# Performance work log

Hardware: AMD Instinct MI355X
Metric: run time of the kernel (lower is better)

The kernel has to match this reference:

```python
import jax, jax.numpy as jnp
import numpy as np

CUBOID = (2, 7, 7)
SHIFT = (1, 3, 3)
NUM_HEADS = 4
LN_EPS = 1e-5


def _cuboid_reorder(data, cs):
    # (B,T,H,W,C) -> (B, num_cuboids, cuboid_volume, C), strategy = ('l','l','l')
    B, T, H, W, C = data.shape
    bt, bh, bw = cs
    d = data.reshape(B, T // bt, bt, H // bh, bh, W // bw, bw, C)
    d = d.transpose(0, 1, 3, 5, 2, 4, 6, 7)
    return d.reshape(B, (T // bt) * (H // bh) * (W // bw), bt * bh * bw, C)


def _cuboid_reorder_reverse(data, cs, shape):
    T, H, W = shape
    bt, bh, bw = cs
    B, _, _, C = data.shape
    d = data.reshape(B, T // bt, H // bh, W // bw, bt, bh, bw, C)
    d = d.transpose(0, 1, 4, 2, 5, 3, 6, 7)
    return d.reshape(B, T, H, W, C)


def _compute_attn_mask(shape, cs, ss):
    # Shift-window mask; no padding needed (dims divisible by cuboid), so the
    # data mask is all-ones and the mask is just the shift-region equality mask.
    T, H, W = shape
    shift_mask = np.zeros((1, T, H, W, 1), np.float32)
    cnt = 0
    for t in (slice(-cs[0]), slice(-cs[0], -ss[0]), slice(-ss[0], None)):
        for h in (slice(-cs[1]), slice(-cs[1], -ss[1]), slice(-ss[1], None)):
            for w in (slice(-cs[2]), slice(-cs[2], -ss[2]), slice(-ss[2], None)):
                shift_mask[:, t, h, w, :] = cnt
                cnt += 1
    sm = _cuboid_reorder(shift_mask, cs)[0, :, :, 0]  # (num_cuboids, vol)
    attn_mask = (sm[:, None, :] - sm[:, :, None]) == 0  # (num_cuboids, vol, vol)
    return jnp.asarray(attn_mask)


def setup_inputs() -> dict:
    key = jax.random.key(0)
    k1, k2, k3 = jax.random.split(key, 3)
    B, T, H, W, C = 2, 16, 56, 56, 128
    return {
        "x": jax.random.normal(k1, (B, T, H, W, C), jnp.float32),
        "gamma": jnp.ones((C,), jnp.float32),
        "beta": jnp.zeros((C,), jnp.float32),
        "w_qkv": jax.random.normal(k2, (C, 3 * C), jnp.float32) * 0.05,
        "w_proj": jax.random.normal(k3, (C, C), jnp.float32) * 0.05,
        "b_proj": jnp.zeros((C,), jnp.float32),
    }


def reference(x, gamma, beta, w_qkv, w_proj, b_proj):
    B, T, H, W, C = x.shape
    hd = C // NUM_HEADS
    scale = hd ** -0.5

    # pre-norm (torch LayerNorm, biased variance)
    mu = jnp.mean(x, axis=-1, keepdims=True)
    var = jnp.var(x, axis=-1, keepdims=True)
    xn = (x - mu) * jax.lax.rsqrt(var + LN_EPS) * gamma + beta

    # shift + cuboid reorder
    shifted = jnp.roll(xn, shift=(-SHIFT[0], -SHIFT[1], -SHIFT[2]), axis=(1, 2, 3))
    r = _cuboid_reorder(shifted, CUBOID)  # (B, nc, vol, C)
    nc, vol = r.shape[1], r.shape[2]

    qkv = (r @ w_qkv).reshape(B, nc, vol, 3, NUM_HEADS, hd)
    q = qkv[..., 0, :, :] * scale  # (B, nc, vol, h, d)
    k = qkv[..., 1, :, :]
    v = qkv[..., 2, :, :]

    attn_score = jnp.einsum("bnihd,bnjhd->bhnij", q, k)  # (B, h, nc, vol, vol)
    mask = _compute_attn_mask((T, H, W), CUBOID, SHIFT)  # (nc, vol, vol)
    attn_score = jnp.where(mask[None, None], attn_score, jnp.float32(-1e18))
    attn = jax.nn.softmax(attn_score, axis=-1) * mask[None, None]

    out = jnp.einsum("bhnij,bnjhd->bnihd", attn, v).reshape(B, nc, vol, C)
    out = out @ w_proj + b_proj

    out = _cuboid_reorder_reverse(out, CUBOID, (T, H, W))
    out = jnp.roll(out, shift=SHIFT, axis=(1, 2, 3))
    return out
```

## Files before the change

### kernel.cpp

```cpp
#include <hip/hip_runtime.h>

typedef short s16x8 __attribute__((ext_vector_type(8)));
typedef float f32x4_t __attribute__((ext_vector_type(4)));

#define VOL 98
#define VPAD 112
#define CH 128
#define NWV 7
#define NTH (NWV * 64)
#define MASKNEG -1e9f

struct Smem {
  unsigned short bufA[VPAD * CH];
  unsigned short vt[CH * CH];
  unsigned short pst[NWV][512];
  unsigned int catbits[27][4];
  int cat[VPAD];
  int gidx[VPAD];
};

__device__ __forceinline__ unsigned short f2bf(float f) {
  unsigned int u = __float_as_uint(f);
  unsigned int r = u + 0x7FFFu + ((u >> 16) & 1u);
  return (unsigned short)(r >> 16);
}
__device__ __forceinline__ unsigned int pk2(float a, float b) {
  return (unsigned int)f2bf(a) | ((unsigned int)f2bf(b) << 16);
}
__device__ __forceinline__ int swz(int row, int colEl, int strideB) {
  return (row * strideB + colEl * 2) ^ ((row & 7) << 4);
}
__device__ __forceinline__ s16x8 ldsRd(const unsigned short* buf, int row, int colEl, int strideB) {
  return *(const s16x8*)((const char*)buf + swz(row, colEl, strideB));
}
__device__ __forceinline__ void ldsWr64(unsigned short* buf, int row, int colEl, int strideB,
                                        unsigned int lo, unsigned int hi) {
  unsigned long long v = (unsigned long long)lo | ((unsigned long long)hi << 32);
  *(unsigned long long*)((char*)buf + swz(row, colEl, strideB)) = v;
}
__device__ __forceinline__ void ldsWr128(unsigned short* buf, int row, int colEl, int strideB, uint4 v) {
  *(uint4*)((char*)buf + swz(row, colEl, strideB)) = v;
}
__device__ __forceinline__ s16x8 u4cast(unsigned a, unsigned b, unsigned c, unsigned d) {
  union { uint4 u; s16x8 v; } cv;
  cv.u = make_uint4(a, b, c, d);
  return cv.v;
}

__global__ void prepack_weights(const float* __restrict__ wqkv,
                                const float* __restrict__ wproj,
                                unsigned short* __restrict__ dst) {
  int lane = threadIdx.x;
  int blk = blockIdx.x;
  if (blk < 96) {
    int ct = blk >> 2, ks = blk & 3;
    int r0 = ks * 32 + ((lane >> 4) << 3);
    int col = ct * 16 + (lane & 15);
    unsigned short* d = dst + (((size_t)(ct * 4 + ks) * 64 + lane) * 8);
#pragma unroll
    for (int j = 0; j < 8; ++j) d[j] = f2bf(wqkv[(size_t)(r0 + j) * 384 + col]);
  } else {
    int bb = blk - 96;
    int ct = bb >> 2, ks = bb & 3;
    int r0 = ks * 32 + ((lane >> 4) << 3);
    int col = ct * 16 + (lane & 15);
    unsigned short* d = dst + 49152 + (((size_t)(ct * 4 + ks) * 64 + lane) * 8);
#pragma unroll
    for (int j = 0; j < 8; ++j) d[j] = f2bf(wproj[(size_t)(r0 + j) * 128 + col]);
  }
}

__global__ __launch_bounds__(NTH, 4) void fused_cuboid_attn(
    const float* __restrict__ x, const float* __restrict__ gamma,
    const float* __restrict__ beta, const float* __restrict__ bproj,
    const unsigned short* __restrict__ wfrag, float* __restrict__ out) {
  __shared__ Smem s;
  const int tid = threadIdx.x;
  const int lane = tid & 63;
  const int itw = tid >> 6;
  const int l15 = lane & 15;
  const int lg = lane >> 4;
  const int lg4 = lg * 4;
  const int lg8 = lg * 8;
  const int bid = blockIdx.x;
  const int b = bid >> 9;
  const int n = bid & 511;
  const int nt = n >> 6, nh = (n >> 3) & 7, nw = n & 7;

  {
    uint4 z = make_uint4(0, 0, 0, 0);
    uint4* pv = (uint4*)s.vt;
    for (int i = tid; i < 2048; i += NTH) pv[i] = z;
    if (tid < 224) ((uint4*)(s.bufA + 98 * CH))[tid] = z;
    if (tid < 27) ((uint4*)s.catbits)[tid] = z;
    if (tid >= NTH - (VPAD - VOL)) s.cat[VOL + tid - (NTH - (VPAD - VOL))] = -1;
  }
  __syncthreads();

  {
    const int grp = tid >> 4;
    const int l = tid & 15;
    const float4 g0 = *(const float4*)(gamma + l * 8);
    const float4 g1 = *(const float4*)(gamma + l * 8 + 4);
    const float4 be0 = *(const float4*)(beta + l * 8);
    const float4 be1 = *(const float4*)(beta + l * 8 + 4);
    for (int i = grp; i < VOL; i += NTH / 16) {
      int dt = (i >= 49) ? 1 : 0;
      int rem = i - dt * 49;
      int dh = (rem * 37) >> 8;
      int dw = rem - dh * 7;
      int t = nt * 2 + dt, h = nh * 7 + dh, w = nw * 7 + dw;
      int ts = (t + 1) & 15;
      int hs = h + 3; if (hs >= 56) hs -= 56;
      int ws2 = w + 3; if (ws2 >= 56) ws2 -= 56;
      int gi = ((b * 16 + ts) * 56 + hs) * 56 + ws2;
      const float* xp = x + (size_t)gi * CH + l * 8;
      float4 v0 = *(const float4*)(xp);
      float4 v1 = *(const float4*)(xp + 4);
      float sum = v0.x + v0.y + v0.z + v0.w + v1.x + v1.y + v1.z + v1.w;
      float ssq = v0.x * v0.x + v0.y * v0.y + v0.z * v0.z + v0.w * v0.w +
                  v1.x * v1.x + v1.y * v1.y + v1.z * v1.z + v1.w * v1.w;
#pragma unroll
      for (int d = 1; d < 16; d <<= 1) {
        sum += __shfl_xor(sum, d);
        ssq += __shfl_xor(ssq, d);
      }
      float mean = sum * (1.0f / 128.0f);
      float var = ssq * (1.0f / 128.0f) - mean * mean;
      float rstd = rsqrtf(var + 1e-5f);
      uint4 pkv;
      pkv.x = pk2((v0.x - mean) * rstd * g0.x + be0.x, (v0.y - mean) * rstd * g0.y + be0.y);
      pkv.y = pk2((v0.z - mean) * rstd * g0.z + be0.z, (v0.w - mean) * rstd * g0.w + be0.w);
      pkv.z = pk2((v1.x - mean) * rstd * g1.x + be1.x, (v1.y - mean) * rstd * g1.y + be1.y);
      pkv.w = pk2((v1.z - mean) * rstd * g1.z + be1.z, (v1.w - mean) * rstd * g1.w + be1.w);
      ldsWr128(s.bufA, i, l * 8, 256, pkv);
      if (l == 0) {
        int tc = (t < 14) ? 0 : ((t < 15) ? 1 : 2);
        int hc = (h < 49) ? 0 : ((h < 53) ? 1 : 2);
        int wc = (w < 49) ? 0 : ((w < 53) ? 1 : 2);
        int c = tc * 9 + hc * 3 + wc;
        s.cat[i] = c;
        s.gidx[i] = gi;
        atomicOr(&s.catbits[c][i >> 5], 1u << (i & 31));
      }
    }
  }
  __syncthreads();

  s16x8 xf[4];
#pragma unroll
  for (int ks = 0; ks < 4; ++ks) xf[ks] = ldsRd(s.bufA, itw * 16 + l15, ks * 32 + lg8, 256);
  __syncthreads();

  unsigned qp[8][2];
  {
    const float QSCALE = (float)(0.17677669529663687 * 1.4426950408889634);
#pragma unroll
    for (int ct = 0; ct < 24; ++ct) {
      const unsigned short* wf = wfrag + ((size_t)ct * 2048 + (size_t)lane * 8);
      s16x8 wv[4];
#pragma unroll
      for (int ks = 0; ks < 4; ++ks) wv[ks] = *(const s16x8*)(wf + ks * 512);
      f32x4_t acc = {0.f, 0.f, 0.f, 0.f};
      if (ct < 16) {
#pragma unroll
        for (int ks = 0; ks < 4; ++ks)
          acc = __builtin_amdgcn_mfma_f32_16x16x32_bf16(wv[ks], xf[ks], acc, 0, 0, 0);
        if (ct < 8) {
          qp[ct][0] = pk2(acc[0] * QSCALE, acc[1] * QSCALE);
          qp[ct][1] = pk2(acc[2] * QSCALE, acc[3] * QSCALE);
        } else {
          ldsWr64(s.bufA, itw * 16 + l15, (ct - 8) * 16 + lg4, 256,
                  pk2(acc[0], acc[1]), pk2(acc[2], acc[3]));
        }
      } else {
#pragma unroll
        for (int ks = 0; ks < 4; ++ks)
          acc = __builtin_amdgcn_mfma_f32_16x16x32_bf16(xf[ks], wv[ks], acc, 0, 0, 0);
        ldsWr64(s.vt, (ct - 16) * 16 + l15, itw * 16 + lg4, 256,
                pk2(acc[0], acc[1]), pk2(acc[2], acc[3]));
      }
    }
  }
  __syncthreads();

  unsigned oreg[4][4];
  {
    unsigned short* ps = s.pst[itw];
    const int q = itw * 16 + l15;
    int cq = s.cat[q]; if (cq < 0) cq = 0;
    const uint4 mwv = *(const uint4*)&s.catbits[cq][0];
    f32x4_t cm[7];
#pragma unroll
    for (int jt = 0; jt < 7; ++jt) {
      unsigned mword = ((jt >> 1) == 0) ? mwv.x : ((jt >> 1) == 1) ? mwv.y
                      : ((jt >> 1) == 2) ? mwv.z : mwv.w;
#pragma unroll
      for (int r = 0; r < 4; ++r)
        cm[jt][r] = ((mword >> ((jt & 1) * 16 + lg4 + r)) & 1u) ? 0.f : MASKNEG;
    }
    const int srcA = ((lg & 1) * 2) * 16 + l15;
    const int srcB = ((lg & 1) * 2 + 1) * 16 + l15;
    const bool hiT = (lg >> 1) != 0;
#pragma unroll
    for (int hh = 0; hh < 4; ++hh) {
      unsigned a0 = __shfl(qp[2 * hh][0], srcA), b0 = __shfl(qp[2 * hh + 1][0], srcA);
      unsigned a1 = __shfl(qp[2 * hh][1], srcA), b1 = __shfl(qp[2 * hh + 1][1], srcA);
      unsigned a2 = __shfl(qp[2 * hh][0], srcB), b2 = __shfl(qp[2 * hh + 1][0], srcB);
      unsigned a3 = __shfl(qp[2 * hh][1], srcB), b3 = __shfl(qp[2 * hh + 1][1], srcB);
      s16x8 qa = u4cast(hiT ? b0 : a0, hiT ? b1 : a1, hiT ? b2 : a2, hiT ? b3 : a3);
      f32x4_t sc[7];
#pragma unroll
      for (int jt = 0; jt < 7; ++jt) {
        s16x8 kb = ldsRd(s.bufA, jt * 16 + l15, hh * 32 + lg8, 256);
        sc[jt] = __builtin_amdgcn_mfma_f32_16x16x32_bf16(kb, qa, cm[jt], 0, 0, 0);
      }
      float m = sc[0][0];
#pragma unroll
      for (int jt = 0; jt < 7; ++jt)
#pragma unroll
        for (int r = 0; r < 4; ++r) m = fmaxf(m, sc[jt][r]);
      m = fmaxf(m, __shfl_xor(m, 16));
      m = fmaxf(m, __shfl_xor(m, 32));
      float ssum = 0.f;
#pragma unroll
      for (int jt = 0; jt < 7; ++jt)
#pragma unroll
        for (int r = 0; r < 4; ++r) {
          float p = exp2f(sc[jt][r] - m);
          sc[jt][r] = p;
          ssum += p;
        }
      ssum += __shfl_xor(ssum, 16);
      ssum += __shfl_xor(ssum, 32);
      float rinv = 1.0f / ssum;
      f32x4_t o0 = {0.f, 0.f, 0.f, 0.f}, o1 = {0.f, 0.f, 0.f, 0.f};
#pragma unroll
      for (int ks = 0; ks < 4; ++ks) {
        const int jtA = 2 * ks, jtB = 2 * ks + 1;
        ldsWr64(ps, l15, lg4, 64, pk2(sc[jtA][0], sc[jtA][1]), pk2(sc[jtA][2], sc[jtA][3]));
        unsigned pb0 = 0, pb1 = 0;
        if (jtB < 7) {
          pb0 = pk2(sc[jtB][0], sc[jtB][1]);
          pb1 = pk2(sc[jtB][2], sc[jtB][3]);
        }
        ldsWr64(ps, l15, 16 + lg4, 64, pb0, pb1);
        asm volatile("" ::: "memory");
        s16x8 pa = ldsRd(ps, l15, lg8, 64);
        s16x8 v0 = ldsRd(s.vt, hh * 32 + l15, ks * 32 + lg8, 256);
        s16x8 v1 = ldsRd(s.vt, hh * 32 + 16 + l15, ks * 32 + lg8, 256);
        o0 = __builtin_amdgcn_mfma_f32_16x16x32_bf16(v0, pa, o0, 0, 0, 0);
        o1 = __builtin_amdgcn_mfma_f32_16x16x32_bf16(v1, pa, o1, 0, 0, 0);
      }
      oreg[hh][0] = pk2(o0[0] * rinv, o0[1] * rinv);
      oreg[hh][1] = pk2(o0[2] * rinv, o0[3] * rinv);
      oreg[hh][2] = pk2(o1[0] * rinv, o1[1] * rinv);
      oreg[hh][3] = pk2(o1[2] * rinv, o1[3] * rinv);
    }
  }
  __syncthreads();

  {
    const int q = itw * 16 + l15;
#pragma unroll
    for (int hh = 0; hh < 4; ++hh) {
      ldsWr64(s.bufA, q, hh * 32 + lg4, 256, oreg[hh][0], oreg[hh][1]);
      ldsWr64(s.bufA, q, hh * 32 + 16 + lg4, 256, oreg[hh][2], oreg[hh][3]);
    }
  }
  __syncthreads();

  {
    const unsigned short* wp = wfrag + 49152;
    s16x8 of[4];
#pragma unroll
    for (int ks = 0; ks < 4; ++ks) of[ks] = ldsRd(s.bufA, itw * 16 + l15, ks * 32 + lg8, 256);
    const int row = itw * 16 + l15;
    const bool valid = row < VOL;
    const size_t gbase = valid ? (size_t)s.gidx[row] * CH : 0;
#pragma unroll
    for (int ct = 0; ct < 8; ++ct) {
      const unsigned short* wf = wp + ((size_t)ct * 2048 + (size_t)lane * 8);
      float4 b4 = *(const float4*)(bproj + ct * 16 + lg4);
      f32x4_t acc = {b4.x, b4.y, b4.z, b4.w};
#pragma unroll
      for (int ks = 0; ks < 4; ++ks) {
        s16x8 wv = *(const s16x8*)(wf + ks * 512);
        acc = __builtin_amdgcn_mfma_f32_16x16x32_bf16(wv, of[ks], acc, 0, 0, 0);
      }
      if (valid) {
        float4 res;
        res.x = acc[0]; res.y = acc[1]; res.z = acc[2]; res.w = acc[3];
        *(float4*)(out + gbase + ct * 16 + lg4) = res;
      }
    }
  }
}

extern "C" void kernel_launch(void* const* d_in, const int* in_sizes, int n_in,
                              void* d_out, int out_size, void* d_ws, size_t ws_size,
                              hipStream_t stream) {
  const float* x = (const float*)d_in[0];
  const float* gamma = (const float*)d_in[1];
  const float* beta = (const float*)d_in[2];
  const float* wqkv = (const float*)d_in[3];
  const float* wproj = (const float*)d_in[4];
  const float* bproj = (const float*)d_in[5];
  float* out = (float*)d_out;
  unsigned short* wsf = (unsigned short*)d_ws;
  (void)in_sizes; (void)n_in; (void)out_size; (void)ws_size;

  prepack_weights<<<128, 64, 0, stream>>>(wqkv, wproj, wsf);
  fused_cuboid_attn<<<1024, NTH, 0, stream>>>(x, gamma, beta, bproj, wsf, out);
}
```

Before: 79.38 us.

## Prefetch input rows before LDS zeroing, cheaper bf16 pack, split softmax reductions

The global loads of x rows and the category/index math are hoisted ahead of the LDS zero-fill and its barrier and held in registers, so load latency overlaps the initialization. The bf16 packing now uses a v_perm with add-0x8000 rounding (round-half-up instead of round-to-nearest-even). The softmax max and sum reductions are split into four independent chains to shorten dependency latency. This raises register pressure from holding the prefetched rows and changes rounding slightly.

```diff
diff --git a/kernel.cpp b/kernel.cpp
--- a/kernel.cpp
+++ b/kernel.cpp
@@ -25,7 +25,13 @@
   return (unsigned short)(r >> 16);
 }
 __device__ __forceinline__ unsigned int pk2(float a, float b) {
+#if __has_builtin(__builtin_amdgcn_perm)
+  return __builtin_amdgcn_perm(__float_as_uint(b) + 0x8000u,
+                               __float_as_uint(a) + 0x8000u,
+                               0x07060302u);
+#else
   return (unsigned int)f2bf(a) | ((unsigned int)f2bf(b) << 16);
+#endif
 }
 __device__ __forceinline__ int swz(int row, int colEl, int strideB) {
   return (row * strideB + colEl * 2) ^ ((row & 7) << 4);
@@ -87,24 +93,14 @@
   const int n = bid & 511;
   const int nt = n >> 6, nh = (n >> 3) & 7, nw = n & 7;
 
-  {
-    uint4 z = make_uint4(0, 0, 0, 0);
-    uint4* pv = (uint4*)s.vt;
-    for (int i = tid; i < 2048; i += NTH) pv[i] = z;
-    if (tid < 224) ((uint4*)(s.bufA + 98 * CH))[tid] = z;
-    if (tid < 27) ((uint4*)s.catbits)[tid] = z;
-    if (tid >= NTH - (VPAD - VOL)) s.cat[VOL + tid - (NTH - (VPAD - VOL))] = -1;
-  }
-  __syncthreads();
-
-  {
-    const int grp = tid >> 4;
-    const int l = tid & 15;
-    const float4 g0 = *(const float4*)(gamma + l * 8);
-    const float4 g1 = *(const float4*)(gamma + l * 8 + 4);
-    const float4 be0 = *(const float4*)(beta + l * 8);
-    const float4 be1 = *(const float4*)(beta + l * 8 + 4);
-    for (int i = grp; i < VOL; i += NTH / 16) {
+  const int grp = tid >> 4;
+  const int l = tid & 15;
+  float4 xv[4][2];
+  int giv[4], catv[4];
+#pragma unroll
+  for (int it2 = 0; it2 < 4; ++it2) {
+    int i = grp + it2 * 28;
+    if (i < VOL) {
       int dt = (i >= 49) ? 1 : 0;
       int rem = i - dt * 49;
       int dh = (rem * 37) >> 8;
@@ -115,33 +111,59 @@
       int ws2 = w + 3; if (ws2 >= 56) ws2 -= 56;
       int gi = ((b * 16 + ts) * 56 + hs) * 56 + ws2;
       const float* xp = x + (size_t)gi * CH + l * 8;
-      float4 v0 = *(const float4*)(xp);
-      float4 v1 = *(const float4*)(xp + 4);
-      float sum = v0.x + v0.y + v0.z + v0.w + v1.x + v1.y + v1.z + v1.w;
-      float ssq = v0.x * v0.x + v0.y * v0.y + v0.z * v0.z + v0.w * v0.w +
-                  v1.x * v1.x + v1.y * v1.y + v1.z * v1.z + v1.w * v1.w;
-#pragma unroll
-      for (int d = 1; d < 16; d <<= 1) {
-        sum += __shfl_xor(sum, d);
-        ssq += __shfl_xor(ssq, d);
-      }
-      float mean = sum * (1.0f / 128.0f);
-      float var = ssq * (1.0f / 128.0f) - mean * mean;
-      float rstd = rsqrtf(var + 1e-5f);
-      uint4 pkv;
-      pkv.x = pk2((v0.x - mean) * rstd * g0.x + be0.x, (v0.y - mean) * rstd * g0.y + be0.y);
-      pkv.y = pk2((v0.z - mean) * rstd * g0.z + be0.z, (v0.w - mean) * rstd * g0.w + be0.w);
-      pkv.z = pk2((v1.x - mean) * rstd * g1.x + be1.x, (v1.y - mean) * rstd * g1.y + be1.y);
-      pkv.w = pk2((v1.z - mean) * rstd * g1.z + be1.z, (v1.w - mean) * rstd * g1.w + be1.w);
-      ldsWr128(s.bufA, i, l * 8, 256, pkv);
-      if (l == 0) {
-        int tc = (t < 14) ? 0 : ((t < 15) ? 1 : 2);
-        int hc = (h < 49) ? 0 : ((h < 53) ? 1 : 2);
-        int wc = (w < 49) ? 0 : ((w < 53) ? 1 : 2);
-        int c = tc * 9 + hc * 3 + wc;
-        s.cat[i] = c;
-        s.gidx[i] = gi;
-        atomicOr(&s.catbits[c][i >> 5], 1u << (i & 31));
+      xv[it2][0] = *(const float4*)(xp);
+      xv[it2][1] = *(const float4*)(xp + 4);
+      giv[it2] = gi;
+      int tc = (t < 14) ? 0 : ((t < 15) ? 1 : 2);
+      int hc = (h < 49) ? 0 : ((h < 53) ? 1 : 2);
+      int wc = (w < 49) ? 0 : ((w < 53) ? 1 : 2);
+      catv[it2] = tc * 9 + hc * 3 + wc;
+    }
+  }
+
+  {
+    uint4 z = make_uint4(0, 0, 0, 0);
+    uint4* pv = (uint4*)s.vt;
+    for (int i = tid; i < 2048; i += NTH) pv[i] = z;
+    if (tid < 224) ((uint4*)(s.bufA + 98 * CH))[tid] = z;
+    if (tid < 27) ((uint4*)s.catbits)[tid] = z;
+    if (tid >= NTH - (VPAD - VOL)) s.cat[VOL + tid - (NTH - (VPAD - VOL))] = -1;
+  }
+  __syncthreads();
+
+  {
+    const float4 g0 = *(const float4*)(gamma + l * 8);
+    const float4 g1 = *(const float4*)(gamma + l * 8 + 4);
+    const float4 be0 = *(const float4*)(beta + l * 8);
+    const float4 be1 = *(const float4*)(beta + l * 8 + 4);
+#pragma unroll
+    for (int it2 = 0; it2 < 4; ++it2) {
+      int i = grp + it2 * 28;
+      if (i < VOL) {
+        float4 v0 = xv[it2][0];
+        float4 v1 = xv[it2][1];
+        float sum = v0.x + v0.y + v0.z + v0.w + v1.x + v1.y + v1.z + v1.w;
+        float ssq = v0.x * v0.x + v0.y * v0.y + v0.z * v0.z + v0.w * v0.w +
+                    v1.x * v1.x + v1.y * v1.y + v1.z * v1.z + v1.w * v1.w;
+#pragma unroll
+        for (int d = 1; d < 16; d <<= 1) {
+          sum += __shfl_xor(sum, d);
+          ssq += __shfl_xor(ssq, d);
+        }
+        float mean = sum * (1.0f / 128.0f);
+        float var = ssq * (1.0f / 128.0f) - mean * mean;
+        float rstd = rsqrtf(var + 1e-5f);
+        uint4 pkv;
+        pkv.x = pk2((v0.x - mean) * rstd * g0.x + be0.x, (v0.y - mean) * rstd * g0.y + be0.y);
+        pkv.y = pk2((v0.z - mean) * rstd * g0.z + be0.z, (v0.w - mean) * rstd * g0.w + be0.w);
+        pkv.z = pk2((v1.x - mean) * rstd * g1.x + be1.x, (v1.y - mean) * rstd * g1.y + be1.y);
+        pkv.w = pk2((v1.z - mean) * rstd * g1.z + be1.z, (v1.w - mean) * rstd * g1.w + be1.w);
+        ldsWr128(s.bufA, i, l * 8, 256, pkv);
+        if (l == 0) {
+          s.cat[i] = catv[it2];
+          s.gidx[i] = giv[it2];
+          atomicOr(&s.catbits[catv[it2]][i >> 5], 1u << (i & 31));
+        }
       }
     }
   }
@@ -215,22 +237,28 @@
         s16x8 kb = ldsRd(s.bufA, jt * 16 + l15, hh * 32 + lg8, 256);
         sc[jt] = __builtin_amdgcn_mfma_f32_16x16x32_bf16(kb, qa, cm[jt], 0, 0, 0);
       }
-      float m = sc[0][0];
-#pragma unroll
-      for (int jt = 0; jt < 7; ++jt)
-#pragma unroll
-        for (int r = 0; r < 4; ++r) m = fmaxf(m, sc[jt][r]);
+      float m0 = sc[0][0], m1 = sc[0][1], m2 = sc[0][2], m3 = sc[0][3];
+#pragma unroll
+      for (int jt = 1; jt < 7; ++jt) {
+        m0 = fmaxf(m0, sc[jt][0]);
+        m1 = fmaxf(m1, sc[jt][1]);
+        m2 = fmaxf(m2, sc[jt][2]);
+        m3 = fmaxf(m3, sc[jt][3]);
+      }
+      float m = fmaxf(fmaxf(m0, m1), fmaxf(m2, m3));
       m = fmaxf(m, __shfl_xor(m, 16));
       m = fmaxf(m, __shfl_xor(m, 32));
-      float ssum = 0.f;
-#pragma unroll
-      for (int jt = 0; jt < 7; ++jt)
-#pragma unroll
-        for (int r = 0; r < 4; ++r) {
-          float p = exp2f(sc[jt][r] - m);
-          sc[jt][r] = p;
-          ssum += p;
-        }
+      float s0 = 0.f, s1 = 0.f, s2 = 0.f, s3 = 0.f;
+#pragma unroll
+      for (int jt = 0; jt < 7; ++jt) {
+        float p0 = exp2f(sc[jt][0] - m);
+        float p1 = exp2f(sc[jt][1] - m);
+        float p2 = exp2f(sc[jt][2] - m);
+        float p3 = exp2f(sc[jt][3] - m);
+        sc[jt][0] = p0; sc[jt][1] = p1; sc[jt][2] = p2; sc[jt][3] = p3;
+        s0 += p0; s1 += p1; s2 += p2; s3 += p3;
+      }
+      float ssum = (s0 + s1) + (s2 + s3);
       ssum += __shfl_xor(ssum, 16);
       ssum += __shfl_xor(ssum, 32);
       float rinv = 1.0f / ssum;
```

After: 74.74 us. 5.9% less time.
